# Performance work log

Measured on AMD Instinct MI355X. Metric: run time of the kernel, lower is better.

The kernel has to match this reference:

```python
import jax, jax.numpy as jnp
import numpy as np

N, E, DIN, D, H, L = 4096, 65536, 128, 256, 4, 3
DH = D // H


def _ln(x, g, b, eps=1e-5):
    m = jnp.mean(x, axis=-1, keepdims=True)
    v = jnp.mean((x - m) ** 2, axis=-1, keepdims=True)
    return (x - m) * jax.lax.rsqrt(v + eps) * g + b


def _gcn(x, w, b, row, col, n):
    # PyG GCNConv: add self-loops, symmetric normalization D^-1/2 A D^-1/2, aggregate at col (target)
    ar = jnp.arange(n, dtype=row.dtype)
    r = jnp.concatenate([row, ar])
    c = jnp.concatenate([col, ar])
    deg = jax.ops.segment_sum(jnp.ones(r.shape[0], x.dtype), c, num_segments=n)
    dinv = jnp.where(deg > 0, deg ** -0.5, 0.0)
    norm = dinv[r] * dinv[c]  # (E+N,)
    msg = x @ w.T  # (N, out)
    return jax.ops.segment_sum(norm[:, None] * msg[r], c, num_segments=n) + b


def setup_inputs() -> dict:
    key = jax.random.key(0)
    ks = jax.random.split(key, 12)
    rnd = lambda i, shape: jax.random.normal(ks[i], shape, jnp.float32) * 0.05
    return {
        "node_features": jax.random.normal(ks[0], (N, DIN), jnp.float32),
        "edge_index": jax.random.randint(ks[1], (2, E), 0, N, jnp.int32),
        "gcn1_w": rnd(2, (D, DIN)), "gcn1_b": jnp.zeros((D,), jnp.float32),
        "gcn2_w": rnd(3, (D, D)), "gcn2_b": jnp.zeros((D,), jnp.float32),
        "edge_w": rnd(4, (H, 3)), "edge_b": jnp.zeros((H,), jnp.float32),
        "proj_w": rnd(5, (D, DIN + D)), "proj_b": jnp.zeros((D,), jnp.float32),
        "wqkv": rnd(6, (L, 3 * D, D)), "bqkv": jnp.zeros((L, 3 * D), jnp.float32),
        "wo": rnd(7, (L, D, D)), "bo": jnp.zeros((L, D), jnp.float32),
        "ffn_w1": rnd(8, (L, 4 * D, D)), "ffn_b1": jnp.zeros((L, 4 * D), jnp.float32),
        "ffn_w2": rnd(9, (L, D, 4 * D)), "ffn_b2": jnp.zeros((L, D), jnp.float32),
        "ln1_g": jnp.ones((L, D), jnp.float32), "ln1_b": jnp.zeros((L, D), jnp.float32),
        "ln2_g": jnp.ones((L, D), jnp.float32), "ln2_b": jnp.zeros((L, D), jnp.float32),
        "out_w": rnd(10, (1, D)), "out_b": jnp.zeros((1,), jnp.float32),
    }


def reference(node_features, edge_index, gcn1_w, gcn1_b, gcn2_w, gcn2_b,
              edge_w, edge_b, proj_w, proj_b, wqkv, bqkv, wo, bo,
              ffn_w1, ffn_b1, ffn_w2, ffn_b2, ln1_g, ln1_b, ln2_g, ln2_b,
              out_w, out_b):
    n = node_features.shape[0]
    row, col = edge_index[0], edge_index[1]
    # two-layer GCN
    h = jax.nn.relu(_gcn(node_features, gcn1_w, gcn1_b, row, col, n))
    g = _gcn(h, gcn2_w, gcn2_b, row, col, n)
    x = jnp.concatenate([node_features, g], axis=-1) @ proj_w.T + proj_b  # (N, D)
    # edge-aware attention bias: per-edge linear+sigmoid scattered into dense (H, N, N)
    feat = jnp.stack([row.astype(x.dtype), col.astype(x.dtype),
                      jnp.ones(row.shape[0], x.dtype)], axis=-1)  # (E, 3)
    bpe = jax.nn.sigmoid(feat @ edge_w.T + edge_b)  # (E, H)
    bias = jnp.zeros((H, n, n), x.dtype).at[:, row, col].set(bpe.T)
    scale = 1.0 / np.sqrt(DH)
    for l in range(L):
        qkv = x @ wqkv[l].T + bqkv[l]
        q, k, v = jnp.split(qkv, 3, axis=-1)
        q = q.reshape(n, H, DH); k = k.reshape(n, H, DH); v = v.reshape(n, H, DH)
        s = jnp.einsum('nhd,mhd->hnm', q, k) * scale + bias
        a = jax.nn.softmax(s, axis=-1)
        o = jnp.einsum('hnm,mhd->nhd', a, v).reshape(n, D) @ wo[l].T + bo[l]
        x = _ln(x + o, ln1_g[l], ln1_b[l])
        f = jax.nn.relu(x @ ffn_w1[l].T + ffn_b1[l]) @ ffn_w2[l].T + ffn_b2[l]
        x = _ln(x + f, ln2_g[l], ln2_b[l])
    return jax.nn.sigmoid(x @ out_w.T + out_b)  # (N, 1) probs
```

## Files before the change

### kernel.cpp

```cpp
#include <hip/hip_runtime.h>
#include <math.h>

#define NN 4096
#define NE 65536
#define DIN 128
#define DM 256
#define NH 4
#define NL 3
#define NCH 4
#define TPC (NN / 64 / NCH)
#define NBKT 16384

typedef __attribute__((ext_vector_type(8))) short bf16x8;
typedef __attribute__((ext_vector_type(4))) float f32x4;

__device__ inline ushort f2b(float f) {
    union { float f; uint u; } v; v.f = f;
    uint r = v.u + 0x7fffu + ((v.u >> 16) & 1u);
    return (ushort)(r >> 16);
}

__device__ inline uint cvt_pk_bf16(float lo, float hi) {
    uint r;
    asm("v_cvt_pk_bf16_f32 %0, %1, %2" : "=v"(r) : "v"(lo), "v"(hi));
    return r;
}

__device__ inline void gl_lds16(const ushort* g, ushort* l) {
    __builtin_amdgcn_global_load_lds(
        (const __attribute__((address_space(1))) void*)g,
        (__attribute__((address_space(3))) void*)l, 16, 0, 0);
}


__global__ void k_edge1(const int* __restrict__ row, const int* __restrict__ col,
                        uint* __restrict__ bitmap, int* __restrict__ cnt_c,
                        int* __restrict__ bcnt, unsigned char* __restrict__ flag) {
    int e = blockIdx.x * 256 + threadIdx.x;
    if (e >= NE) return;
    int r = row[e], c = col[e];
    atomicAdd(&cnt_c[c], 1);
    uint idx = (uint)r * 4096u + (uint)c;
    uint m = 1u << (idx & 31);
    uint old = atomicOr(&bitmap[idx >> 5], m);
    int isnew = (old & m) ? 0 : 1;
    flag[e] = (unsigned char)isnew;
    if (isnew) atomicAdd(&bcnt[(r >> 4) * 64 + (c >> 6)], 1);
}

__global__ void k_edge2(const int* __restrict__ row, const int* __restrict__ col,
                        const unsigned char* __restrict__ flag,
                        const int* __restrict__ sc, int* __restrict__ fc, int* __restrict__ csc_row,
                        const int* __restrict__ bstart, int* __restrict__ bfill,
                        uint* __restrict__ entcomb,
                        const float* __restrict__ ew, const float* __restrict__ eb) {
    int e = blockIdx.x * 256 + threadIdx.x;
    if (e >= NE) return;
    int r = row[e], c = col[e];
    csc_row[sc[c] + atomicAdd(&fc[c], 1)] = r;
    if (flag[e]) {
        int key = (r >> 4) * 64 + (c >> 6);
        int pos = bstart[key] + atomicAdd(&bfill[key], 1);
        uint idx = (uint)(((r & 15) << 6) | (c & 63));
        float fr = (float)r, fc2 = (float)c;
#pragma unroll
        for (int h = 0; h < NH; ++h) {
            float arg = ew[h * 3 + 0] * fr + ew[h * 3 + 1] * fc2 + ew[h * 3 + 2] + eb[h];
            float sig = 1.f / (1.f + __expf(-arg));
            entcomb[(long)h * NE + pos] = idx | ((uint)f2b(sig) << 16);
        }
    }
}

template <int N>
__global__ void k_scan(const int* __restrict__ cnt, int* __restrict__ start) {
    __shared__ int part[256];
    const int C = N / 256;
    int t = threadIdx.x;
    int s = 0;
    for (int i = 0; i < C; ++i) s += cnt[t * C + i];
    part[t] = s;
    __syncthreads();
    if (t == 0) {
        int acc = 0;
        for (int i = 0; i < 256; ++i) { int v = part[i]; part[i] = acc; acc += v; }
        start[N] = acc;
    }
    __syncthreads();
    int acc = part[t];
    for (int i = 0; i < C; ++i) { start[t * C + i] = acc; acc += cnt[t * C + i]; }
}

__global__ void k_dinv(const int* __restrict__ cnt_c, float* __restrict__ dinv) {
    int i = blockIdx.x * 256 + threadIdx.x;
    if (i < NN) dinv[i] = 1.0f / sqrtf((float)(cnt_c[i] + 1));
}

struct CvtP { const float* s[8]; ushort* d[8]; int n[8]; };
__global__ void k_cvt(CvtP p) {
    int y = blockIdx.y;
    int base = (blockIdx.x * 256 + threadIdx.x) * 4;
    if (base >= p.n[y]) return;
    float4 v = *(const float4*)(p.s[y] + base);
    float sc = 1.f;
    if (y == 1 && ((base >> 8) % 768) < 256) sc = 0.125f;
    ushort4 o;
    o.x = f2b(v.x * sc); o.y = f2b(v.y * sc); o.z = f2b(v.z * sc); o.w = f2b(v.w * sc);
    *(ushort4*)(p.d[y] + base) = o;
}

__global__ void k_scaleb(const float* __restrict__ b, float* __restrict__ o) {
    int i = blockIdx.x * 256 + threadIdx.x;
    if (i < NL * 768) o[i] = b[i] * (((i % 768) < 256) ? 0.125f : 1.f);
}

template <int FLAGS>
__global__ __launch_bounds__(256) void k_gemm_b(
    const ushort* __restrict__ A, int lda,
    const ushort* __restrict__ B, int ldb,
    float* __restrict__ Cf, ushort* __restrict__ Cb, ushort* __restrict__ Cb2, int ldc,
    int K, const float* __restrict__ bias, const float* __restrict__ gsrc) {
    __shared__ ushort As[128 * 64];
    __shared__ ushort Bs[128 * 64];
    const int tid = threadIdx.x;
    const int w = tid >> 6, l = tid & 63;
    const int l15 = l & 15, l4 = l >> 4;
    const int row0 = blockIdx.y * 128, col0 = blockIdx.x * 128;
    const int wm = (w >> 1) * 64, wn = (w & 1) * 64;
    f32x4 acc[4][4];
#pragma unroll
    for (int i = 0; i < 4; ++i)
#pragma unroll
        for (int j = 0; j < 4; ++j) acc[i][j] = (f32x4){0.f, 0.f, 0.f, 0.f};
    for (int k0 = 0; k0 < K; k0 += 64) {
#pragma unroll
        for (int i = 0; i < 4; ++i) {
            int ci = tid + 256 * i;
            int r = ci >> 3, s = ci & 7;
            if (FLAGS & 32) {
                if (k0 < 128) {
                    gl_lds16(A + (long)(row0 + r) * DIN + k0 + ((s ^ (r & 7)) * 8), &As[ci * 8]);
                } else {
                    const float* gp = gsrc + (long)(row0 + r) * DM + (k0 - 128) + s * 8;
                    float4 v0 = *(const float4*)(gp);
                    float4 v1 = *(const float4*)(gp + 4);
                    union { bf16x8 v; ushort u[8]; } pk;
                    pk.u[0] = f2b(v0.x); pk.u[1] = f2b(v0.y); pk.u[2] = f2b(v0.z); pk.u[3] = f2b(v0.w);
                    pk.u[4] = f2b(v1.x); pk.u[5] = f2b(v1.y); pk.u[6] = f2b(v1.z); pk.u[7] = f2b(v1.w);
                    *(bf16x8*)&As[r * 64 + ((s ^ (r & 7)) * 8)] = pk.v;
                }
            } else {
                gl_lds16(A + (long)(row0 + r) * lda + k0 + ((s ^ (r & 7)) * 8), &As[ci * 8]);
            }
            gl_lds16(B + (long)(col0 + r) * ldb + k0 + ((s ^ (r & 7)) * 8), &Bs[ci * 8]);
        }
        __syncthreads();
#pragma unroll
        for (int kk = 0; kk < 2; ++kk) {
            bf16x8 af[4], bfr[4];
#pragma unroll
            for (int i = 0; i < 4; ++i) {
                int ar = wm + i * 16 + l15;
                af[i] = *(const bf16x8*)&As[ar * 64 + (((kk * 4 + l4) ^ (ar & 7)) * 8)];
                int br = wn + i * 16 + l15;
                bfr[i] = *(const bf16x8*)&Bs[br * 64 + (((kk * 4 + l4) ^ (br & 7)) * 8)];
            }
#pragma unroll
            for (int i = 0; i < 4; ++i)
#pragma unroll
                for (int j = 0; j < 4; ++j)
                    acc[i][j] = __builtin_amdgcn_mfma_f32_16x16x32_bf16(af[i], bfr[j], acc[i][j], 0, 0, 0);
        }
        __syncthreads();
    }
#pragma unroll
    for (int i = 0; i < 4; ++i)
#pragma unroll
        for (int j = 0; j < 4; ++j) {
            int rb = row0 + wm + i * 16;
            int cb = col0 + wn + j * 16 + l15;
            float bv = bias ? bias[cb] : 0.f;
            if (FLAGS & 16) {
                if (cb < 512) {
#pragma unroll
                    for (int q = 0; q < 4; ++q)
                        Cb[(long)(rb + l4 * 4 + q) * 512 + cb] = f2b(acc[i][j][q] + bv);
                } else {
                    ushort4 o4;
                    o4.x = f2b(acc[i][j][0] + bv);
                    o4.y = f2b(acc[i][j][1] + bv);
                    o4.z = f2b(acc[i][j][2] + bv);
                    o4.w = f2b(acc[i][j][3] + bv);
                    *(ushort4*)(Cb2 + (long)(cb - 512) * NN + rb + l4 * 4) = o4;
                }
            } else if (FLAGS & 8) {
                ushort4 o4;
                o4.x = f2b(acc[i][j][0] + bv);
                o4.y = f2b(acc[i][j][1] + bv);
                o4.z = f2b(acc[i][j][2] + bv);
                o4.w = f2b(acc[i][j][3] + bv);
                *(ushort4*)(Cb + (long)cb * ldc + rb + l4 * 4) = o4;
            } else {
#pragma unroll
                for (int q = 0; q < 4; ++q) {
                    int r = rb + l4 * 4 + q;
                    float v = acc[i][j][q] + bv;
                    if (FLAGS & 4) v = fmaxf(v, 0.f);
                    if (FLAGS & 1) Cf[(long)r * ldc + cb] = v;
                    if (FLAGS & 2) Cb[(long)r * ldc + cb] = f2b(v);
                }
            }
        }
}

template <int COMB>
__global__ __launch_bounds__(256) void k_gemm_ln(
    const ushort* __restrict__ A, int lda,
    const ushort* __restrict__ B, int ldb, int K,
    const float* __restrict__ bias,
    float* __restrict__ x, ushort* __restrict__ xb,
    const float* __restrict__ gam, const float* __restrict__ bet,
    const float* __restrict__ opart, const float2* __restrict__ ml) {
    __shared__ ushort As[16 * 64];
    __shared__ ushort Bs[256 * 64];
    __shared__ float red[4][16][2];
    const int tid = threadIdx.x;
    const int w = tid >> 6, l = tid & 63;
    const int l15 = l & 15, l4 = l >> 4;
    const int row0 = blockIdx.x * 16;
    f32x4 acc[4];
#pragma unroll
    for (int j = 0; j < 4; ++j) acc[j] = (f32x4){0.f, 0.f, 0.f, 0.f};
    for (int k0 = 0; k0 < K; k0 += 64) {
        if (tid < 128) {
            int r = tid >> 3, s = tid & 7;
            if (COMB) {
                int row = row0 + r;
                int h = k0 >> 6;
                float2 m0 = ml[(0 * (long)NH + h) * NN + row];
                float2 m1 = ml[(1 * (long)NH + h) * NN + row];
                float2 m2 = ml[(2 * (long)NH + h) * NN + row];
                float2 m3 = ml[(3 * (long)NH + h) * NN + row];
                float M = fmaxf(fmaxf(m0.x, m1.x), fmaxf(m2.x, m3.x));
                float e0 = __expf(m0.x - M), e1 = __expf(m1.x - M);
                float e2 = __expf(m2.x - M), e3 = __expf(m3.x - M);
                float inv = 1.f / (m0.y * e0 + m1.y * e1 + m2.y * e2 + m3.y * e3);
                int d0 = s * 8;
                const float* p0 = opart + ((0 * (long)NH + h) * NN + row) * 64 + d0;
                const float* p1 = opart + ((1 * (long)NH + h) * NN + row) * 64 + d0;
                const float* p2 = opart + ((2 * (long)NH + h) * NN + row) * 64 + d0;
                const float* p3 = opart + ((3 * (long)NH + h) * NN + row) * 64 + d0;
                union { bf16x8 v; ushort u[8]; } pk;
#pragma unroll
                for (int j = 0; j < 8; ++j) {
                    float ov = e0 * p0[j] + e1 * p1[j] + e2 * p2[j] + e3 * p3[j];
                    pk.u[j] = f2b(ov * inv);
                }
                *(bf16x8*)&As[r * 64 + ((s ^ (r & 7)) * 8)] = pk.v;
            } else {
                gl_lds16(A + (long)(row0 + r) * lda + k0 + ((s ^ (r & 7)) * 8), &As[tid * 8]);
            }
        }
#pragma unroll
        for (int i = 0; i < 8; ++i) {
            int idx = i * 256 + tid;
            int r = idx >> 3, s = idx & 7;
            gl_lds16(B + (long)r * ldb + k0 + ((s ^ (r & 7)) * 8), &Bs[idx * 8]);
        }
        __syncthreads();
#pragma unroll
        for (int kk = 0; kk < 2; ++kk) {
            bf16x8 af = *(const bf16x8*)&As[l15 * 64 + (((kk * 4 + l4) ^ (l15 & 7)) * 8)];
#pragma unroll
            for (int j = 0; j < 4; ++j) {
                int br = w * 64 + j * 16 + l15;
                bf16x8 bfr = *(const bf16x8*)&Bs[br * 64 + (((kk * 4 + l4) ^ (br & 7)) * 8)];
                acc[j] = __builtin_amdgcn_mfma_f32_16x16x32_bf16(af, bfr, acc[j], 0, 0, 0);
            }
        }
        __syncthreads();
    }
    float val[4][4];
#pragma unroll
    for (int j = 0; j < 4; ++j) {
        int c = w * 64 + j * 16 + l15;
        float bv = bias[c];
#pragma unroll
        for (int q = 0; q < 4; ++q) {
            int r = row0 + l4 * 4 + q;
            val[j][q] = acc[j][q] + bv + x[(long)r * DM + c];
        }
    }
    float sum[4], sq[4];
#pragma unroll
    for (int q = 0; q < 4; ++q) {
        sum[q] = (val[0][q] + val[1][q]) + (val[2][q] + val[3][q]);
        sq[q] = (val[0][q] * val[0][q] + val[1][q] * val[1][q]) +
                (val[2][q] * val[2][q] + val[3][q] * val[3][q]);
    }
#pragma unroll
    for (int o = 1; o < 16; o <<= 1)
#pragma unroll
        for (int q = 0; q < 4; ++q) {
            sum[q] += __shfl_xor(sum[q], o);
            sq[q] += __shfl_xor(sq[q], o);
        }
    if (l15 == 0)
#pragma unroll
        for (int q = 0; q < 4; ++q) {
            red[w][l4 * 4 + q][0] = sum[q];
            red[w][l4 * 4 + q][1] = sq[q];
        }
    __syncthreads();
    float mean[4], rs[4];
#pragma unroll
    for (int q = 0; q < 4; ++q) {
        int rl = l4 * 4 + q;
        float ts = (red[0][rl][0] + red[1][rl][0]) + (red[2][rl][0] + red[3][rl][0]);
        float tq = (red[0][rl][1] + red[1][rl][1]) + (red[2][rl][1] + red[3][rl][1]);
        float m = ts * (1.f / 256.f);
        float var = tq * (1.f / 256.f) - m * m;
        mean[q] = m;
        rs[q] = rsqrtf(var + 1e-5f);
    }
#pragma unroll
    for (int j = 0; j < 4; ++j) {
        int c = w * 64 + j * 16 + l15;
        float gv = gam[c], bv = bet[c];
#pragma unroll
        for (int q = 0; q < 4; ++q) {
            int r = row0 + l4 * 4 + q;
            float ov = (val[j][q] - mean[q]) * rs[q] * gv + bv;
            x[(long)r * DM + c] = ov;
            xb[(long)r * DM + c] = f2b(ov);
        }
    }
}

template <int ACT, int B16>
__global__ void k_gcn_agg(const float* __restrict__ msg, const int* __restrict__ sc,
                          const int* __restrict__ csc_row, const float* __restrict__ dinv,
                          const float* __restrict__ bias,
                          float* __restrict__ outf, ushort* __restrict__ outb) {
    int j = blockIdx.x;
    int d = threadIdx.x;
    float acc = 0.f;
    int a = sc[j], b = sc[j + 1];
    for (int i = a; i < b; ++i) {
        int r = csc_row[i];
        acc += dinv[r] * msg[(long)r * DM + d];
    }
    float dj = dinv[j];
    float v = dj * acc + dj * dj * msg[(long)j * DM + d] + bias[d];
    if (ACT) v = fmaxf(v, 0.f);
    if (B16) outb[(long)j * DM + d] = f2b(v);
    else outf[(long)j * DM + d] = v;
}

__global__ __launch_bounds__(256, 4) void k_attn(
    const ushort* __restrict__ qkb, const ushort* __restrict__ vT,
    const int* __restrict__ bstart, const uint* __restrict__ entcomb,
    float* __restrict__ opart, float2* __restrict__ ml) {
    __shared__ ushort Klds[2][4096];
    __shared__ ushort Vlds[2][4096];
    __shared__ ushort Pl[4096];
    const int qb = blockIdx.x, h = blockIdx.y, cz = blockIdx.z;
    const int tid = threadIdx.x, w = tid >> 6, l = tid & 63;
    const int l15 = l & 15, l4 = l >> 4;
    bf16x8 qf[2];
    {
        const ushort* qp = qkb + (long)(qb * 64 + w * 16 + l15) * 512 + h * 64 + l4 * 8;
        qf[0] = *(const bf16x8*)(qp);
        qf[1] = *(const bf16x8*)(qp + 32);
    }
    const ushort* Kb = qkb + 256 + h * 64;
    const ushort* Vb = vT + (long)(h * 64) * NN;
    const uint* ec = entcomb + (long)h * NE;
    f32x4 o[4];
#pragma unroll
    for (int f = 0; f < 4; ++f) o[f] = (f32x4){0.f, 0.f, 0.f, 0.f};
    float m_run = -1e30f, l_run = 0.f;
    char* P = (char*)&Pl[w * 1024];
    const int bktW = (qb * 4 + w) * 64;
    const int t0 = cz * TPC;

    auto stage = [&](int b, int t) {
#pragma unroll
        for (int i = 0; i < 2; ++i) {
            int idx = i * 256 + tid;
            int r = idx >> 3, sl = idx & 7;
            gl_lds16(Kb + (long)(t * 64 + r) * 512 + ((sl ^ (r & 7)) * 8),
                     &Klds[b][idx * 8]);
            gl_lds16(Vb + (long)r * NN + t * 64 + ((sl ^ (r & 7)) * 8),
                     &Vlds[b][idx * 8]);
        }
    };

    int bs_c = bstart[bktW + t0], be_c = bstart[bktW + t0 + 1];
    stage(0, t0);
    int cur = 0;
    for (int tt = 0; tt < TPC; ++tt) {
        const int t = t0 + tt;
        asm volatile("s_waitcnt lgkmcnt(0)" ::: "memory");
        __builtin_amdgcn_s_barrier();
        int bs_n = 0, be_n = 0;
        if (tt + 1 < TPC) {
            stage(cur ^ 1, t + 1);
            bs_n = bstart[bktW + t + 1];
            be_n = bstart[bktW + t + 2];
            asm volatile("s_waitcnt vmcnt(4)" ::: "memory");
        } else {
            asm volatile("s_waitcnt vmcnt(0)" ::: "memory");
        }
        __builtin_amdgcn_sched_barrier(0);
        __builtin_amdgcn_s_barrier();
        __builtin_amdgcn_sched_barrier(0);

        const ushort* Kl = Klds[cur];
        const ushort* Vl = Vlds[cur];
        f32x4 s4[4];
#pragma unroll
        for (int f = 0; f < 4; ++f) {
            int kc = f * 16 + l15;
            bf16x8 k0 = *(const bf16x8*)&Kl[kc * 64 + ((l4 ^ (kc & 7)) * 8)];
            bf16x8 k1 = *(const bf16x8*)&Kl[kc * 64 + (((4 + l4) ^ (kc & 7)) * 8)];
            f32x4 a = (f32x4){0.f, 0.f, 0.f, 0.f};
            a = __builtin_amdgcn_mfma_f32_16x16x32_bf16(k0, qf[0], a, 0, 0, 0);
            a = __builtin_amdgcn_mfma_f32_16x16x32_bf16(k1, qf[1], a, 0, 0, 0);
            s4[f] = a;
        }
        for (int i = bs_c; i < be_c; ++i) {
            uint e = ec[i];
            int r4 = (e >> 6) & 15, c6 = e & 63;
            if (l15 == r4 && ((c6 >> 2) & 3) == l4) {
                union { uint u; float f; } sv;
                sv.u = e & 0xFFFF0000u;
                float sig = sv.f;
                switch (((c6 >> 4) << 2) | (c6 & 3)) {
                    case 0:  s4[0][0] += sig; break; case 1:  s4[0][1] += sig; break;
                    case 2:  s4[0][2] += sig; break; case 3:  s4[0][3] += sig; break;
                    case 4:  s4[1][0] += sig; break; case 5:  s4[1][1] += sig; break;
                    case 6:  s4[1][2] += sig; break; case 7:  s4[1][3] += sig; break;
                    case 8:  s4[2][0] += sig; break; case 9:  s4[2][1] += sig; break;
                    case 10: s4[2][2] += sig; break; case 11: s4[2][3] += sig; break;
                    case 12: s4[3][0] += sig; break; case 13: s4[3][1] += sig; break;
                    case 14: s4[3][2] += sig; break; case 15: s4[3][3] += sig; break;
                }
            }
        }
        float ma = fmaxf(fmaxf(s4[0][0], s4[0][1]), fmaxf(s4[0][2], s4[0][3]));
        float mb = fmaxf(fmaxf(s4[1][0], s4[1][1]), fmaxf(s4[1][2], s4[1][3]));
        float mc = fmaxf(fmaxf(s4[2][0], s4[2][1]), fmaxf(s4[2][2], s4[2][3]));
        float md = fmaxf(fmaxf(s4[3][0], s4[3][1]), fmaxf(s4[3][2], s4[3][3]));
        float me = fmaxf(fmaxf(ma, mb), fmaxf(mc, md));
        me = fmaxf(me, __shfl_xor(me, 16));
        me = fmaxf(me, __shfl_xor(me, 32));
        if (!__all(me <= m_run + 8.f)) {
            float mn = fmaxf(m_run, me);
            float fac = __expf(m_run - mn);
            m_run = mn;
            l_run *= fac;
#pragma unroll
            for (int f = 0; f < 4; ++f)
#pragma unroll
                for (int r = 0; r < 4; ++r) o[f][r] *= fac;
        }
        float rp[4];
#pragma unroll
        for (int f = 0; f < 4; ++f) {
            float p0 = __expf(s4[f][0] - m_run);
            float p1 = __expf(s4[f][1] - m_run);
            float p2 = __expf(s4[f][2] - m_run);
            float p3 = __expf(s4[f][3] - m_run);
            s4[f][0] = p0; s4[f][1] = p1; s4[f][2] = p2; s4[f][3] = p3;
            rp[f] = (p0 + p1) + (p2 + p3);
        }
        float rsum = (rp[0] + rp[1]) + (rp[2] + rp[3]);
        rsum += __shfl_xor(rsum, 16);
        rsum += __shfl_xor(rsum, 32);
        l_run += rsum;
#pragma unroll
        for (int f = 0; f < 4; ++f)
#pragma unroll
            for (int p = 0; p < 2; ++p) {
                uint u = cvt_pk_bf16(s4[f][2 * p], s4[f][2 * p + 1]);
                int slot = f * 2 + (l4 >> 1);
                int byte = l15 * 128 + ((slot ^ (l15 & 7)) << 4) + (l4 & 1) * 8 + p * 4;
                *(uint*)(P + byte) = u;
            }
        asm volatile("s_waitcnt lgkmcnt(0)" ::: "memory");
        __builtin_amdgcn_sched_barrier(0);
#pragma unroll
        for (int ks = 0; ks < 2; ++ks) {
            bf16x8 pb = *(const bf16x8*)(P + l15 * 128 + (((ks * 4 + l4) ^ (l15 & 7)) << 4));
#pragma unroll
            for (int fd = 0; fd < 4; ++fd) {
                int d = fd * 16 + l15;
                bf16x8 vfr = *(const bf16x8*)&Vl[d * 64 + (((ks * 4 + l4) ^ (d & 7)) * 8)];
                o[fd] = __builtin_amdgcn_mfma_f32_16x16x32_bf16(vfr, pb, o[fd], 0, 0, 0);
            }
        }
        bs_c = bs_n; be_c = be_n;
        cur ^= 1;
    }
    long base = (((long)cz * NH + h) * NN + qb * 64 + w * 16 + l15) * 64;
#pragma unroll
    for (int fd = 0; fd < 4; ++fd)
#pragma unroll
        for (int r = 0; r < 4; ++r)
            opart[base + fd * 16 + l4 * 4 + r] = o[fd][r];
    if (l4 == 0)
        ml[((long)cz * NH + h) * NN + qb * 64 + w * 16 + l15] = make_float2(m_run, l_run);
}


__global__ void k_out(const float* __restrict__ x, const float* __restrict__ w,
                      const float* __restrict__ b, float* __restrict__ out) {
    int row = blockIdx.x;
    int lane = threadIdx.x;
    float s = 0.f;
#pragma unroll
    for (int i = 0; i < 4; ++i) s += x[(long)row * DM + lane + 64 * i] * w[lane + 64 * i];
#pragma unroll
    for (int o = 1; o < 64; o <<= 1) s += __shfl_xor(s, o);
    if (lane == 0) out[row] = 1.f / (1.f + expf(-(s + b[0])));
}

__global__ void k_sentinel(float* out, int n) {
    int i = blockIdx.x * 256 + threadIdx.x;
    if (i < n) out[i] = 1.0e9f;
}


extern "C" void kernel_launch(void* const* d_in, const int* in_sizes, int n_in,
                              void* d_out, int out_size, void* d_ws, size_t ws_size,
                              hipStream_t stream) {
    const float* nf = (const float*)d_in[0];
    const int* ei = (const int*)d_in[1];
    const int* erow = ei;
    const int* ecol = ei + NE;
    const float* gcn1_w = (const float*)d_in[2];
    const float* gcn1_b = (const float*)d_in[3];
    const float* gcn2_w = (const float*)d_in[4];
    const float* gcn2_b = (const float*)d_in[5];
    const float* edge_w = (const float*)d_in[6];
    const float* edge_b = (const float*)d_in[7];
    const float* proj_w = (const float*)d_in[8];
    const float* proj_b = (const float*)d_in[9];
    const float* wqkv = (const float*)d_in[10];
    const float* bqkv = (const float*)d_in[11];
    const float* wo = (const float*)d_in[12];
    const float* bo = (const float*)d_in[13];
    const float* ffn_w1 = (const float*)d_in[14];
    const float* ffn_b1 = (const float*)d_in[15];
    const float* ffn_w2 = (const float*)d_in[16];
    const float* ffn_b2 = (const float*)d_in[17];
    const float* ln1_g = (const float*)d_in[18];
    const float* ln1_b = (const float*)d_in[19];
    const float* ln2_g = (const float*)d_in[20];
    const float* ln2_b = (const float*)d_in[21];
    const float* out_w = (const float*)d_in[22];
    const float* out_b = (const float*)d_in[23];
    float* out = (float*)d_out;

    char* wp = (char*)d_ws;
    size_t off = 0;
    auto alloc = [&](size_t bytes) -> void* {
        void* p = wp + off;
        off = (off + bytes + 255) & ~(size_t)255;
        return p;
    };
    char* big = (char*)alloc((size_t)NCH * NH * NN * 64 * 4);
    float* msg = (float*)big;
    float* opart = (float*)big;
    ushort* ffnHb = (ushort*)big;
    float* x = (float*)alloc((size_t)NN * DM * 4);
    ushort* xb = (ushort*)alloc((size_t)NN * DM * 2);
    ushort* hb = (ushort*)alloc((size_t)NN * DM * 2);
    float* g = (float*)alloc((size_t)NN * DM * 4);
    ushort* qkb = (ushort*)alloc((size_t)NN * 512 * 2);
    ushort* vT = (ushort*)alloc((size_t)DM * NN * 2);
    float2* ml = (float2*)alloc((size_t)NCH * NH * NN * 8);
    ushort* nfb = (ushort*)alloc((size_t)NN * DIN * 2);
    ushort* wqkvb = (ushort*)alloc((size_t)NL * 768 * DM * 2);
    ushort* wob = (ushort*)alloc((size_t)NL * DM * DM * 2);
    ushort* f1b = (ushort*)alloc((size_t)NL * 1024 * DM * 2);
    ushort* f2bw = (ushort*)alloc((size_t)NL * DM * 1024 * 2);
    ushort* g1b = (ushort*)alloc((size_t)DM * DIN * 2);
    ushort* g2b = (ushort*)alloc((size_t)DM * DM * 2);
    ushort* pjb = (ushort*)alloc((size_t)DM * 384 * 2);
    float* bq2 = (float*)alloc((size_t)NL * 768 * 4);
    uint* bitmap = (uint*)alloc((size_t)NN * NN / 8);
    unsigned char* flag = (unsigned char*)alloc(NE);
    int* cnt_c = (int*)alloc((size_t)NN * 4);
    int* bcnt = (int*)alloc((size_t)NBKT * 4);
    int* sc = (int*)alloc((size_t)(NN + 1) * 4);
    int* bstart = (int*)alloc((size_t)(NBKT + 1) * 4);
    int* fc = (int*)alloc((size_t)NN * 4);
    int* bfill = (int*)alloc((size_t)NBKT * 4);
    int* csc_row = (int*)alloc((size_t)NE * 4);
    uint* entcomb = (uint*)alloc((size_t)NH * NE * 4);
    float* dinv = (float*)alloc((size_t)NN * 4);

    if (off > ws_size) {
        k_sentinel<<<(out_size + 255) / 256, 256, 0, stream>>>(out, out_size);
        return;
    }

    hipMemsetAsync(bitmap, 0, (size_t)NN * NN / 8, stream);
    hipMemsetAsync(cnt_c, 0, NN * 4, stream);
    hipMemsetAsync(bcnt, 0, NBKT * 4, stream);
    hipMemsetAsync(fc, 0, NN * 4, stream);
    hipMemsetAsync(bfill, 0, NBKT * 4, stream);
    k_edge1<<<NE / 256, 256, 0, stream>>>(erow, ecol, bitmap, cnt_c, bcnt, flag);
    k_scan<NN><<<1, 256, 0, stream>>>(cnt_c, sc);
    k_scan<NBKT><<<1, 256, 0, stream>>>(bcnt, bstart);
    k_edge2<<<NE / 256, 256, 0, stream>>>(erow, ecol, flag, sc, fc, csc_row, bstart, bfill,
                                          entcomb, edge_w, edge_b);
    k_dinv<<<NN / 256, 256, 0, stream>>>(cnt_c, dinv);

    CvtP cp;
    cp.s[0] = nf;      cp.d[0] = nfb;   cp.n[0] = NN * DIN;
    cp.s[1] = wqkv;    cp.d[1] = wqkvb; cp.n[1] = NL * 768 * DM;
    cp.s[2] = wo;      cp.d[2] = wob;   cp.n[2] = NL * DM * DM;
    cp.s[3] = ffn_w1;  cp.d[3] = f1b;   cp.n[3] = NL * 1024 * DM;
    cp.s[4] = ffn_w2;  cp.d[4] = f2bw;  cp.n[4] = NL * DM * 1024;
    cp.s[5] = gcn1_w;  cp.d[5] = g1b;   cp.n[5] = DM * DIN;
    cp.s[6] = gcn2_w;  cp.d[6] = g2b;   cp.n[6] = DM * DM;
    cp.s[7] = proj_w;  cp.d[7] = pjb;   cp.n[7] = DM * 384;
    k_cvt<<<dim3(768, 8), 256, 0, stream>>>(cp);
    k_scaleb<<<(NL * 768 + 255) / 256, 256, 0, stream>>>(bqkv, bq2);

    k_gemm_b<1><<<dim3(DM / 128, NN / 128), 256, 0, stream>>>(
        nfb, DIN, g1b, DIN, msg, nullptr, nullptr, DM, DIN, nullptr, nullptr);
    k_gcn_agg<1, 1><<<NN, DM, 0, stream>>>(msg, sc, csc_row, dinv, gcn1_b, nullptr, hb);
    k_gemm_b<1><<<dim3(DM / 128, NN / 128), 256, 0, stream>>>(
        hb, DM, g2b, DM, msg, nullptr, nullptr, DM, DM, nullptr, nullptr);
    k_gcn_agg<0, 0><<<NN, DM, 0, stream>>>(msg, sc, csc_row, dinv, gcn2_b, g, nullptr);
    k_gemm_b<35><<<dim3(DM / 128, NN / 128), 256, 0, stream>>>(
        nfb, DIN, pjb, 384, x, xb, nullptr, DM, 384, proj_b, g);

    for (int l = 0; l < NL; ++l) {
        k_gemm_b<18><<<dim3(768 / 128, NN / 128), 256, 0, stream>>>(
            xb, DM, wqkvb + (long)l * 768 * DM, DM, nullptr, qkb, vT, 512, DM,
            bq2 + (long)l * 768, nullptr);
        k_attn<<<dim3(NN / 64, NH, NCH), 256, 0, stream>>>(
            qkb, vT, bstart, entcomb, opart, ml);
        k_gemm_ln<1><<<NN / 16, 256, 0, stream>>>(
            nullptr, DM, wob + (long)l * DM * DM, DM, DM, bo + (long)l * DM,
            x, xb, ln1_g + (long)l * DM, ln1_b + (long)l * DM, opart, ml);
        k_gemm_b<6><<<dim3(1024 / 128, NN / 128), 256, 0, stream>>>(
            xb, DM, f1b + (long)l * 1024 * DM, DM, nullptr, ffnHb, nullptr, 1024, DM,
            ffn_b1 + (long)l * 1024, nullptr);
        k_gemm_ln<0><<<NN / 16, 256, 0, stream>>>(
            ffnHb, 1024, f2bw + (long)l * DM * 1024, 1024, 1024, ffn_b2 + (long)l * DM,
            x, xb, ln2_g + (long)l * DM, ln2_b + (long)l * DM, nullptr, nullptr);
    }
    k_out<<<NN, 64, 0, stream>>>(x, out_w, out_b, out);
}
```

Before: 464.2 us.

## Process two query groups per wave in attention and double split-K chunks

Each attention wave now computes scores and outputs for two 16-row query groups against each staged K/V tile, so each block covers 128 queries and reuses K/V loads. The split over key chunks is doubled to keep the grid size the same, and the partial-softmax combine in the output GEMM is generalized to any chunk count. This raises register use per wave and doubles the partial-output traffic read by the combine.

```diff
diff --git a/kernel.cpp b/kernel.cpp
--- a/kernel.cpp
+++ b/kernel.cpp
@@ -7,7 +7,7 @@
 #define DM 256
 #define NH 4
 #define NL 3
-#define NCH 4
+#define NCH 8
 #define TPC (NN / 64 / NCH)
 #define NBKT 16384
 
@@ -237,23 +237,29 @@
             if (COMB) {
                 int row = row0 + r;
                 int h = k0 >> 6;
-                float2 m0 = ml[(0 * (long)NH + h) * NN + row];
-                float2 m1 = ml[(1 * (long)NH + h) * NN + row];
-                float2 m2 = ml[(2 * (long)NH + h) * NN + row];
-                float2 m3 = ml[(3 * (long)NH + h) * NN + row];
-                float M = fmaxf(fmaxf(m0.x, m1.x), fmaxf(m2.x, m3.x));
-                float e0 = __expf(m0.x - M), e1 = __expf(m1.x - M);
-                float e2 = __expf(m2.x - M), e3 = __expf(m3.x - M);
-                float inv = 1.f / (m0.y * e0 + m1.y * e1 + m2.y * e2 + m3.y * e3);
+                float2 mm[NCH];
+                float M = -1e30f;
+#pragma unroll
+                for (int c = 0; c < NCH; ++c) {
+                    mm[c] = ml[((long)c * NH + h) * NN + row];
+                    M = fmaxf(M, mm[c].x);
+                }
+                float ee[NCH];
+                float den = 0.f;
+#pragma unroll
+                for (int c = 0; c < NCH; ++c) {
+                    ee[c] = __expf(mm[c].x - M);
+                    den += mm[c].y * ee[c];
+                }
+                float inv = 1.f / den;
                 int d0 = s * 8;
-                const float* p0 = opart + ((0 * (long)NH + h) * NN + row) * 64 + d0;
-                const float* p1 = opart + ((1 * (long)NH + h) * NN + row) * 64 + d0;
-                const float* p2 = opart + ((2 * (long)NH + h) * NN + row) * 64 + d0;
-                const float* p3 = opart + ((3 * (long)NH + h) * NN + row) * 64 + d0;
                 union { bf16x8 v; ushort u[8]; } pk;
 #pragma unroll
                 for (int j = 0; j < 8; ++j) {
-                    float ov = e0 * p0[j] + e1 * p1[j] + e2 * p2[j] + e3 * p3[j];
+                    float ov = 0.f;
+#pragma unroll
+                    for (int c = 0; c < NCH; ++c)
+                        ov += ee[c] * opart[(((long)c * NH + h) * NN + row) * 64 + d0 + j];
                     pk.u[j] = f2b(ov * inv);
                 }
                 *(bf16x8*)&As[r * 64 + ((s ^ (r & 7)) * 8)] = pk.v;
@@ -367,21 +373,26 @@
     const int qb = blockIdx.x, h = blockIdx.y, cz = blockIdx.z;
     const int tid = threadIdx.x, w = tid >> 6, l = tid & 63;
     const int l15 = l & 15, l4 = l >> 4;
-    bf16x8 qf[2];
-    {
-        const ushort* qp = qkb + (long)(qb * 64 + w * 16 + l15) * 512 + h * 64 + l4 * 8;
-        qf[0] = *(const bf16x8*)(qp);
-        qf[1] = *(const bf16x8*)(qp + 32);
+    bf16x8 qf[2][2];
+#pragma unroll
+    for (int g = 0; g < 2; ++g) {
+        const ushort* qp = qkb + (long)(qb * 128 + w * 32 + g * 16 + l15) * 512 + h * 64 + l4 * 8;
+        qf[g][0] = *(const bf16x8*)(qp);
+        qf[g][1] = *(const bf16x8*)(qp + 32);
     }
     const ushort* Kb = qkb + 256 + h * 64;
     const ushort* Vb = vT + (long)(h * 64) * NN;
     const uint* ec = entcomb + (long)h * NE;
-    f32x4 o[4];
-#pragma unroll
-    for (int f = 0; f < 4; ++f) o[f] = (f32x4){0.f, 0.f, 0.f, 0.f};
-    float m_run = -1e30f, l_run = 0.f;
+    f32x4 oA[4], oB[4];
+#pragma unroll
+    for (int f = 0; f < 4; ++f) {
+        oA[f] = (f32x4){0.f, 0.f, 0.f, 0.f};
+        oB[f] = (f32x4){0.f, 0.f, 0.f, 0.f};
+    }
+    float mA = -1e30f, lA = 0.f, mB = -1e30f, lB = 0.f;
     char* P = (char*)&Pl[w * 1024];
-    const int bktW = (qb * 4 + w) * 64;
+    const int bktA = (qb * 8 + w * 2) * 64;
+    const int bktB = bktA + 64;
     const int t0 = cz * TPC;
 
     auto stage = [&](int b, int t) {
@@ -396,40 +407,9 @@
         }
     };
 
-    int bs_c = bstart[bktW + t0], be_c = bstart[bktW + t0 + 1];
-    stage(0, t0);
-    int cur = 0;
-    for (int tt = 0; tt < TPC; ++tt) {
-        const int t = t0 + tt;
-        asm volatile("s_waitcnt lgkmcnt(0)" ::: "memory");
-        __builtin_amdgcn_s_barrier();
-        int bs_n = 0, be_n = 0;
-        if (tt + 1 < TPC) {
-            stage(cur ^ 1, t + 1);
-            bs_n = bstart[bktW + t + 1];
-            be_n = bstart[bktW + t + 2];
-            asm volatile("s_waitcnt vmcnt(4)" ::: "memory");
-        } else {
-            asm volatile("s_waitcnt vmcnt(0)" ::: "memory");
-        }
-        __builtin_amdgcn_sched_barrier(0);
-        __builtin_amdgcn_s_barrier();
-        __builtin_amdgcn_sched_barrier(0);
-
-        const ushort* Kl = Klds[cur];
-        const ushort* Vl = Vlds[cur];
-        f32x4 s4[4];
-#pragma unroll
-        for (int f = 0; f < 4; ++f) {
-            int kc = f * 16 + l15;
-            bf16x8 k0 = *(const bf16x8*)&Kl[kc * 64 + ((l4 ^ (kc & 7)) * 8)];
-            bf16x8 k1 = *(const bf16x8*)&Kl[kc * 64 + (((4 + l4) ^ (kc & 7)) * 8)];
-            f32x4 a = (f32x4){0.f, 0.f, 0.f, 0.f};
-            a = __builtin_amdgcn_mfma_f32_16x16x32_bf16(k0, qf[0], a, 0, 0, 0);
-            a = __builtin_amdgcn_mfma_f32_16x16x32_bf16(k1, qf[1], a, 0, 0, 0);
-            s4[f] = a;
-        }
-        for (int i = bs_c; i < be_c; ++i) {
+    auto half = [&](f32x4 (&s4)[4], int bs, int be, float& m_run, float& l_run,
+                    f32x4 (&o)[4], const ushort* Vl, int t) {
+        for (int i = bs; i < be; ++i) {
             uint e = ec[i];
             int r4 = (e >> 6) & 15, c6 = e & 63;
             if (l15 == r4 && ((c6 >> 2) & 3) == l4) {
@@ -500,17 +480,65 @@
                 o[fd] = __builtin_amdgcn_mfma_f32_16x16x32_bf16(vfr, pb, o[fd], 0, 0, 0);
             }
         }
-        bs_c = bs_n; be_c = be_n;
+    };
+
+    int bsA = bstart[bktA + t0], beA = bstart[bktA + t0 + 1];
+    int bsB = bstart[bktB + t0], beB = bstart[bktB + t0 + 1];
+    stage(0, t0);
+    int cur = 0;
+    for (int tt = 0; tt < TPC; ++tt) {
+        const int t = t0 + tt;
+        asm volatile("s_waitcnt lgkmcnt(0)" ::: "memory");
+        __builtin_amdgcn_s_barrier();
+        int bsA_n = 0, beA_n = 0, bsB_n = 0, beB_n = 0;
+        if (tt + 1 < TPC) {
+            stage(cur ^ 1, t + 1);
+            bsA_n = bstart[bktA + t + 1];
+            beA_n = bstart[bktA + t + 2];
+            bsB_n = bstart[bktB + t + 1];
+            beB_n = bstart[bktB + t + 2];
+            asm volatile("s_waitcnt vmcnt(4)" ::: "memory");
+        } else {
+            asm volatile("s_waitcnt vmcnt(0)" ::: "memory");
+        }
+        __builtin_amdgcn_sched_barrier(0);
+        __builtin_amdgcn_s_barrier();
+        __builtin_amdgcn_sched_barrier(0);
+
+        const ushort* Kl = Klds[cur];
+        const ushort* Vl = Vlds[cur];
+        f32x4 sA[4], sB[4];
+#pragma unroll
+        for (int f = 0; f < 4; ++f) {
+            int kc = f * 16 + l15;
+            bf16x8 k0 = *(const bf16x8*)&Kl[kc * 64 + ((l4 ^ (kc & 7)) * 8)];
+            bf16x8 k1 = *(const bf16x8*)&Kl[kc * 64 + (((4 + l4) ^ (kc & 7)) * 8)];
+            f32x4 a = (f32x4){0.f, 0.f, 0.f, 0.f};
+            a = __builtin_amdgcn_mfma_f32_16x16x32_bf16(k0, qf[0][0], a, 0, 0, 0);
+            a = __builtin_amdgcn_mfma_f32_16x16x32_bf16(k1, qf[0][1], a, 0, 0, 0);
+            sA[f] = a;
+            f32x4 b = (f32x4){0.f, 0.f, 0.f, 0.f};
+            b = __builtin_amdgcn_mfma_f32_16x16x32_bf16(k0, qf[1][0], b, 0, 0, 0);
+            b = __builtin_amdgcn_mfma_f32_16x16x32_bf16(k1, qf[1][1], b, 0, 0, 0);
+            sB[f] = b;
+        }
+        half(sA, bsA, beA, mA, lA, oA, Vl, t);
+        half(sB, bsB, beB, mB, lB, oB, Vl, t);
+        bsA = bsA_n; beA = beA_n; bsB = bsB_n; beB = beB_n;
         cur ^= 1;
     }
-    long base = (((long)cz * NH + h) * NN + qb * 64 + w * 16 + l15) * 64;
+    long base0 = (((long)cz * NH + h) * NN + qb * 128 + w * 32 + l15) * 64;
 #pragma unroll
     for (int fd = 0; fd < 4; ++fd)
 #pragma unroll
-        for (int r = 0; r < 4; ++r)
-            opart[base + fd * 16 + l4 * 4 + r] = o[fd][r];
-    if (l4 == 0)
-        ml[((long)cz * NH + h) * NN + qb * 64 + w * 16 + l15] = make_float2(m_run, l_run);
+        for (int r = 0; r < 4; ++r) {
+            opart[base0 + fd * 16 + l4 * 4 + r] = oA[fd][r];
+            opart[base0 + 16 * 64 + fd * 16 + l4 * 4 + r] = oB[fd][r];
+        }
+    if (l4 == 0) {
+        ml[((long)cz * NH + h) * NN + qb * 128 + w * 32 + l15] = make_float2(mA, lA);
+        ml[((long)cz * NH + h) * NN + qb * 128 + w * 32 + 16 + l15] = make_float2(mB, lB);
+    }
 }
 
 
@@ -644,7 +672,7 @@
         k_gemm_b<18><<<dim3(768 / 128, NN / 128), 256, 0, stream>>>(
             xb, DM, wqkvb + (long)l * 768 * DM, DM, nullptr, qkb, vT, 512, DM,
             bq2 + (long)l * 768, nullptr);
-        k_attn<<<dim3(NN / 64, NH, NCH), 256, 0, stream>>>(
+        k_attn<<<dim3(NN / 128, NH, NCH), 256, 0, stream>>>(
             qkb, vT, bstart, entcomb, opart, ml);
         k_gemm_ln<1><<<NN / 16, 256, 0, stream>>>(
             nullptr, DM, wob + (long)l * DM * DM, DM, DM, bo + (long)l * DM,
```

Measured after the change: 471.2 us. No clear change (+1.5%).
